# Optimization experiments

Measured on AMD Instinct MI355X. Metric: run time of the kernel, lower is better.

Reference implementation:

```python
import jax, jax.numpy as jnp
import numpy as np

N = 50000
E = 800000
IN = 128
H = 256


def _sage_conv(x, src, dst, W_l, b_l, W_r, n_nodes):
    # PyG SAGEConv (aggr='mean'): out = lin_l(mean_{j in N(i)} x_j) + lin_r(x_i)
    msg = x[src]                                             # [E, d] gather
    agg = jax.ops.segment_sum(msg, dst, num_segments=n_nodes)  # [N, d]
    cnt = jax.ops.segment_sum(jnp.ones((src.shape[0],), x.dtype), dst,
                              num_segments=n_nodes)
    agg = agg / jnp.maximum(cnt, 1.0)[:, None]               # scatter-mean
    return agg @ W_l + b_l + x @ W_r


def setup_inputs() -> dict:
    key = jax.random.key(0)
    ks = jax.random.split(key, 12)
    s_in, s_h, s_h2 = 1.0 / np.sqrt(IN), 1.0 / np.sqrt(H), 1.0 / np.sqrt(H // 2)
    return {
        "x": jax.random.normal(ks[0], (N, IN), jnp.float32),
        "edge_index": jax.random.randint(ks[1], (2, E), 0, N, dtype=jnp.int32),
        # conv1: in -> H
        "W1_l": jax.random.uniform(ks[2], (IN, H), jnp.float32, -s_in, s_in),
        "b1_l": jnp.zeros((H,), jnp.float32),
        "W1_r": jax.random.uniform(ks[3], (IN, H), jnp.float32, -s_in, s_in),
        # conv2: H -> H
        "W2_l": jax.random.uniform(ks[4], (H, H), jnp.float32, -s_h, s_h),
        "b2_l": jnp.zeros((H,), jnp.float32),
        "W2_r": jax.random.uniform(ks[5], (H, H), jnp.float32, -s_h, s_h),
        # risk head: H -> H//2 -> 1
        "Wh1": jax.random.uniform(ks[6], (H, H // 2), jnp.float32, -s_h, s_h),
        "bh1": jax.random.uniform(ks[7], (H // 2,), jnp.float32, -s_h, s_h),
        "Wh2": jax.random.uniform(ks[8], (H // 2, 1), jnp.float32, -s_h2, s_h2),
        "bh2": jax.random.uniform(ks[9], (1,), jnp.float32, -s_h2, s_h2),
    }


def reference(x, edge_index, W1_l, b1_l, W1_r, W2_l, b2_l, W2_r,
              Wh1, bh1, Wh2, bh2):
    src, dst = edge_index[0], edge_index[1]
    h = jax.nn.relu(_sage_conv(x, src, dst, W1_l, b1_l, W1_r, N))
    h = jax.nn.relu(_sage_conv(h, src, dst, W2_l, b2_l, W2_r, N))
    # risk head (dropout is identity in inference)
    h = jax.nn.relu(h @ Wh1 + bh1)
    return jax.nn.sigmoid(h @ Wh2 + bh2)            # [N, 1]
```

## Files before the change

### kernel.cpp

```cpp
#include <hip/hip_runtime.h>
#include <cstdint>
#include <cstddef>

#define N_NODES 50000
#define N_EDGES 800000
#define DIM_IN 128
#define DIM_H 256
#define CAP 64

using u16 = unsigned short;
using u32 = unsigned int;
using u8 = unsigned char;

typedef __attribute__((ext_vector_type(8))) short bf16x8;
typedef __attribute__((ext_vector_type(4))) float f32x4;
typedef __attribute__((ext_vector_type(2))) float f32x2;

__device__ __forceinline__ u16 f2bf(float x) {
    u32 u = __float_as_uint(x);
    u32 r = (u + 0x7fffu + ((u >> 16) & 1u)) >> 16;
    return (u16)r;
}

__device__ __forceinline__ u8 enc1_sw(float f) {
    u32 u = __float_as_uint(f);
    u32 s = (u >> 24) & 0x80u;
    u32 a = u & 0x7fffffffu;
    if (a >= 0x43e00000u) return (u8)(s | 0x7e);
    if (a < 0x3c800000u) return (u8)s;
    u32 r = a + 0x7ffffu + ((a >> 20) & 1u);
    u32 e8 = (r >> 23) - 120u;
    if (e8 >= 16u) return (u8)(s | 0x7e);
    return (u8)(s | (e8 << 3) | ((r >> 20) & 7u));
}

__device__ __forceinline__ u32 enc4(float f0, float f1, float f2, float f3) {
#if __has_builtin(__builtin_amdgcn_cvt_pk_fp8_f32)
    int w = __builtin_amdgcn_cvt_pk_fp8_f32(f0, f1, 0, false);
    w = __builtin_amdgcn_cvt_pk_fp8_f32(f2, f3, w, true);
    return (u32)w;
#else
    return (u32)enc1_sw(f0) | ((u32)enc1_sw(f1) << 8) |
           ((u32)enc1_sw(f2) << 16) | ((u32)enc1_sw(f3) << 24);
#endif
}

__device__ __forceinline__ u8 enc1(float f) {
#if __has_builtin(__builtin_amdgcn_cvt_pk_fp8_f32)
    return (u8)(__builtin_amdgcn_cvt_pk_fp8_f32(f, 0.f, 0, false) & 0xff);
#else
    return enc1_sw(f);
#endif
}

__device__ __forceinline__ void dec_u32(float* o, u32 w) {
#if __has_builtin(__builtin_amdgcn_cvt_pk_f32_fp8)
    f32x2 a = __builtin_amdgcn_cvt_pk_f32_fp8(w, false);
    f32x2 b = __builtin_amdgcn_cvt_pk_f32_fp8(w, true);
    o[0] = a[0]; o[1] = a[1]; o[2] = b[0]; o[3] = b[1];
#else
    #pragma unroll
    for (int k = 0; k < 4; ++k) {
        u32 x = (w >> (8 * k)) & 0xffu;
        u32 bits = ((x & 0x80u) << 24) | ((x & 0x7fu) << 20);
        o[k] = __uint_as_float(bits) * __uint_as_float(0x7b800000u);
    }
#endif
}

__device__ __forceinline__ void gld_lds16(const u16* g, u16* l) {
    __builtin_amdgcn_global_load_lds(
        (__attribute__((address_space(1))) void*)g,
        (__attribute__((address_space(3))) void*)l, 16, 0, 0);
}

__global__ void fill_bucket(const int* __restrict__ src, const int* __restrict__ dst,
                            int* __restrict__ cnt, int* __restrict__ csr, int e) {
    int i = blockIdx.x * blockDim.x + threadIdx.x;
    if (i < e) {
        int d = dst[i];
        int slot = atomicAdd(&cnt[d], 1);
        if (slot < CAP) csr[d * CAP + slot] = src[i];
    }
}

__global__ __launch_bounds__(256) void prep(
    const float* __restrict__ x,
    const float* __restrict__ W1_l, const float* __restrict__ W1_r,
    const float* __restrict__ W2_l, const float* __restrict__ W2_r,
    const float* __restrict__ Wh1,
    u16* __restrict__ x_hi, u32* __restrict__ x_f8,
    u16* __restrict__ w1l, u16* __restrict__ w1r,
    u16* __restrict__ w2l, u16* __restrict__ w2r, u16* __restrict__ wh1,
    int* __restrict__ cnt) {
    int b = blockIdx.x, tid = threadIdx.x;
    if (b < 49) {
        int i = b * 256 + tid;
        if (i < 12500) reinterpret_cast<int4*>(cnt)[i] = make_int4(0, 0, 0, 0);
        return;
    }
    b -= 49;
    if (b < 6250) {
        int i = b * 256 + tid;
        float4 v = reinterpret_cast<const float4*>(x)[i];
        ushort4 h;
        h.x = f2bf(v.x); h.y = f2bf(v.y); h.z = f2bf(v.z); h.w = f2bf(v.w);
        reinterpret_cast<ushort4*>(x_hi)[i] = h;
        x_f8[i] = enc4(v.x, v.y, v.z, v.w);
        return;
    }
    b -= 6250;
    if (b < 128) {
        int idx = b * 256 + tid; int m = idx >> 7, k = idx & 127;
        w1l[idx] = f2bf(W1_l[(size_t)k * 256 + m]); return;
    }
    b -= 128;
    if (b < 128) {
        int idx = b * 256 + tid; int m = idx >> 7, k = idx & 127;
        w1r[idx] = f2bf(W1_r[(size_t)k * 256 + m]); return;
    }
    b -= 128;
    if (b < 256) {
        int idx = b * 256 + tid; int m = idx >> 8, k = idx & 255;
        w2l[idx] = f2bf(W2_l[(size_t)k * 256 + m]); return;
    }
    b -= 256;
    if (b < 256) {
        int idx = b * 256 + tid; int m = idx >> 8, k = idx & 255;
        w2r[idx] = f2bf(W2_r[(size_t)k * 256 + m]); return;
    }
    b -= 256;
    {
        int idx = b * 256 + tid; int m = idx >> 8, k = idx & 255;
        wh1[idx] = f2bf(Wh1[(size_t)k * 128 + m]);
    }
}

__device__ __forceinline__ void acc16_add(float* acc, uint4 a) {
    float t[4];
    dec_u32(t, a.x); acc[0] += t[0]; acc[1] += t[1]; acc[2] += t[2]; acc[3] += t[3];
    dec_u32(t, a.y); acc[4] += t[0]; acc[5] += t[1]; acc[6] += t[2]; acc[7] += t[3];
    dec_u32(t, a.z); acc[8] += t[0]; acc[9] += t[1]; acc[10] += t[2]; acc[11] += t[3];
    dec_u32(t, a.w); acc[12] += t[0]; acc[13] += t[1]; acc[14] += t[2]; acc[15] += t[3];
}

template <int U4ROW>
__global__ __launch_bounds__(256) void aggregate_f8(
    const uint4* __restrict__ tab, const int* __restrict__ cnt,
    const int* __restrict__ csr, u16* __restrict__ out_hi, int n_nodes) {
    constexpr int EPI = 64 / U4ROW;
    constexpr int D = U4ROW * 16;
    const int lane = threadIdx.x & 63;
    const int v = blockIdx.x * 4 + (threadIdx.x >> 6);
    if (v >= n_nodes) return;
    const int q = lane & (U4ROW - 1);
    const int e = lane / U4ROW;
    const int d = cnt[v];
    const int dl = min(d, CAP);
    const int myidx = (lane < dl) ? csr[v * CAP + lane] : 0;
    float acc[16] = {};
    int j = 0;
    for (; j + 2 * EPI <= dl; j += 2 * EPI) {
        int i0 = __shfl(myidx, j + e, 64);
        int i1 = __shfl(myidx, j + EPI + e, 64);
        uint4 a = tab[(size_t)i0 * U4ROW + q];
        uint4 b = tab[(size_t)i1 * U4ROW + q];
        acc16_add(acc, a);
        acc16_add(acc, b);
    }
    for (; j + EPI <= dl; j += EPI) {
        int i0 = __shfl(myidx, j + e, 64);
        uint4 a = tab[(size_t)i0 * U4ROW + q];
        acc16_add(acc, a);
    }
    int r = dl - j;
    if (r > 0) {
        int ee = (e < r) ? e : 0;
        int i0 = __shfl(myidx, j + ee, 64);
        uint4 a = tab[(size_t)i0 * U4ROW + q];
        if (e < r) acc16_add(acc, a);
    }
    #pragma unroll
    for (int s = U4ROW; s < 64; s <<= 1)
        #pragma unroll
        for (int i = 0; i < 16; ++i) acc[i] += __shfl_xor(acc[i], s, 64);
    const float inv = 1.f / (float)((d > 0) ? d : 1);
    if (e == 0) {
        u32 w[8];
        #pragma unroll
        for (int k = 0; k < 8; ++k) {
            float m0 = acc[2 * k] * inv, m1 = acc[2 * k + 1] * inv;
            w[k] = ((u32)f2bf(m1) << 16) | f2bf(m0);
        }
        u16* dp = out_hi + (size_t)v * D + q * 16;
        *reinterpret_cast<uint4*>(dp) = *reinterpret_cast<uint4*>(&w[0]);
        *reinterpret_cast<uint4*>(dp + 8) = *reinterpret_cast<uint4*>(&w[4]);
    }
}

template <int MODE>
__global__ __launch_bounds__(512) void gemm_fused(
    const u16* __restrict__ Ah1, const u16* __restrict__ Ah2,
    const u16* __restrict__ Bh1, const u16* __restrict__ Bh2,
    const float* __restrict__ bias,
    const u16* __restrict__ wh1t, const float* __restrict__ bh1,
    const float* __restrict__ wh2, const float* __restrict__ bh2,
    u16* __restrict__ Chi, u8* __restrict__ Cf8, float* __restrict__ outF,
    int nrows, int K) {
    __shared__ u16 SMEM[(MODE == 1) ? 37888 : 12288];
    u16* As = SMEM;
    u16* Bs = SMEM + 4096;

    const int tid = threadIdx.x;
    const int lane = tid & 63;
    const int w = tid >> 6;
    const int wr = w >> 2, wc = w & 3;
    const int row0 = blockIdx.x * 128;

    const u16* const Aph[2] = {Ah1, Ah2};
    const u16* const Bph[2] = {Bh1, Bh2};

    f32x4 zero4 = {0.f, 0.f, 0.f, 0.f};
    f32x4 acc[4][4];
    #pragma unroll
    for (int i = 0; i < 4; ++i)
        #pragma unroll
        for (int j = 0; j < 4; ++j) acc[i][j] = zero4;

    const int srow = lane >> 2;
    const int schunk = (lane & 3) * 8;

    const int nks = K >> 5;
    for (int ph = 0; ph < 2; ++ph) {
        const u16* Ab = Aph[ph];
        const u16* Bb = Bph[ph];
        for (int kk = 0; kk < nks; ++kk) {
            #pragma unroll
            for (int t = 0; t < 3; ++t) {
                int slab = w * 3 + t;
                if (slab < 8) {
                    int grow = row0 + slab * 16 + srow;
                    if (grow > nrows - 1) grow = nrows - 1;
                    gld_lds16(Ab + (size_t)grow * K + kk * 32 + schunk,
                              As + slab * 512);
                } else {
                    int gcol = (slab - 8) * 16 + srow;
                    gld_lds16(Bb + (size_t)gcol * K + kk * 32 + schunk,
                              Bs + (slab - 8) * 512);
                }
            }
            __syncthreads();
            bf16x8 af[4], bfr[4];
            #pragma unroll
            for (int i = 0; i < 4; ++i)
                af[i] = *reinterpret_cast<const bf16x8*>(
                    &As[(wr * 64 + i * 16 + (lane & 15)) * 32 + (lane >> 4) * 8]);
            #pragma unroll
            for (int j = 0; j < 4; ++j)
                bfr[j] = *reinterpret_cast<const bf16x8*>(
                    &Bs[(wc * 64 + j * 16 + (lane & 15)) * 32 + (lane >> 4) * 8]);
            #pragma unroll
            for (int i = 0; i < 4; ++i)
                #pragma unroll
                for (int j = 0; j < 4; ++j)
                    acc[i][j] = __builtin_amdgcn_mfma_f32_16x16x32_bf16(
                        af[i], bfr[j], acc[i][j], 0, 0, 0);
            __syncthreads();
        }
    }

    if (MODE == 0) {
        #pragma unroll
        for (int i = 0; i < 4; ++i) {
            #pragma unroll
            for (int j = 0; j < 4; ++j) {
                int col = wc * 64 + j * 16 + (lane & 15);
                float b = bias[col];
                #pragma unroll
                for (int r = 0; r < 4; ++r) {
                    int row = row0 + wr * 64 + i * 16 + (lane >> 4) * 4 + r;
                    if (row < nrows) {
                        float v = fmaxf(acc[i][j][r] + b, 0.f);
                        Chi[(size_t)row * 256 + col] = f2bf(v);
                        Cf8[(size_t)row * 256 + col] = enc1(v);
                    }
                }
            }
        }
    } else {
        char* hb = (char*)SMEM;
        #pragma unroll
        for (int i = 0; i < 4; ++i)
            #pragma unroll
            for (int j = 0; j < 4; ++j) {
                int col = wc * 64 + j * 16 + (lane & 15);
                float b = bias[col];
                #pragma unroll
                for (int r = 0; r < 4; ++r) {
                    int row = wr * 64 + i * 16 + (lane >> 4) * 4 + r;
                    float v = fmaxf(acc[i][j][r] + b, 0.f);
                    int byt = row * 512 + col * 2;
                    *(u16*)(hb + (byt ^ ((row & 7) << 4))) = f2bf(v);
                }
            }
        __syncthreads();

        u16* Bs2 = SMEM + 32768;
        float* hpart = (float*)(SMEM + 32768 + 4096);
        const int whr = wr, whc = wc;
        f32x4 acc2[4][2];
        #pragma unroll
        for (int i = 0; i < 4; ++i) {
            acc2[i][0] = zero4; acc2[i][1] = zero4;
        }
        for (int kk = 0; kk < 8; ++kk) {
            {
                int gcol = w * 16 + srow;
                gld_lds16(wh1t + (size_t)gcol * 256 + kk * 32 + schunk,
                          Bs2 + w * 512);
            }
            __syncthreads();
            bf16x8 af2[4], bfr2[2];
            #pragma unroll
            for (int i = 0; i < 4; ++i) {
                int row = whr * 64 + i * 16 + (lane & 15);
                int byt = row * 512 + kk * 64 + (lane >> 4) * 16;
                af2[i] = *reinterpret_cast<const bf16x8*>(hb + (byt ^ ((row & 7) << 4)));
            }
            #pragma unroll
            for (int j = 0; j < 2; ++j)
                bfr2[j] = *reinterpret_cast<const bf16x8*>(
                    &Bs2[(whc * 32 + j * 16 + (lane & 15)) * 32 + (lane >> 4) * 8]);
            #pragma unroll
            for (int i = 0; i < 4; ++i)
                #pragma unroll
                for (int j = 0; j < 2; ++j)
                    acc2[i][j] = __builtin_amdgcn_mfma_f32_16x16x32_bf16(
                        af2[i], bfr2[j], acc2[i][j], 0, 0, 0);
            __syncthreads();
        }

        float pr[4][4];
        #pragma unroll
        for (int i = 0; i < 4; ++i)
            #pragma unroll
            for (int r = 0; r < 4; ++r) pr[i][r] = 0.f;
        #pragma unroll
        for (int j = 0; j < 2; ++j) {
            int col = whc * 32 + j * 16 + (lane & 15);
            float b1 = bh1[col];
            float wv = wh2[col];
            #pragma unroll
            for (int i = 0; i < 4; ++i)
                #pragma unroll
                for (int r = 0; r < 4; ++r)
                    pr[i][r] += fmaxf(acc2[i][j][r] + b1, 0.f) * wv;
        }
        #pragma unroll
        for (int i = 0; i < 4; ++i)
            #pragma unroll
            for (int r = 0; r < 4; ++r) {
                float s = pr[i][r];
                s += __shfl_xor(s, 1, 64);
                s += __shfl_xor(s, 2, 64);
                s += __shfl_xor(s, 4, 64);
                s += __shfl_xor(s, 8, 64);
                pr[i][r] = s;
            }
        if ((lane & 15) == 0) {
            #pragma unroll
            for (int i = 0; i < 4; ++i)
                #pragma unroll
                for (int r = 0; r < 4; ++r)
                    hpart[whc * 128 + whr * 64 + i * 16 + (lane >> 4) * 4 + r] = pr[i][r];
        }
        __syncthreads();
        if (tid < 128) {
            int row = row0 + tid;
            if (row < nrows) {
                float s = hpart[tid] + hpart[128 + tid] + hpart[256 + tid]
                        + hpart[384 + tid] + bh2[0];
                outF[row] = 1.f / (1.f + expf(-s));
            }
        }
    }
}

static inline size_t align256(size_t x) { return (x + 255) & ~(size_t)255; }

extern "C" void kernel_launch(void* const* d_in, const int* in_sizes, int n_in,
                              void* d_out, int out_size, void* d_ws, size_t ws_size,
                              hipStream_t stream) {
    const float* x    = (const float*)d_in[0];
    const int* ei     = (const int*)d_in[1];
    const float* W1_l = (const float*)d_in[2];
    const float* b1_l = (const float*)d_in[3];
    const float* W1_r = (const float*)d_in[4];
    const float* W2_l = (const float*)d_in[5];
    const float* b2_l = (const float*)d_in[6];
    const float* W2_r = (const float*)d_in[7];
    const float* Wh1  = (const float*)d_in[8];
    const float* bh1  = (const float*)d_in[9];
    const float* Wh2  = (const float*)d_in[10];
    const float* bh2  = (const float*)d_in[11];
    float* out = (float*)d_out;

    const int* src = ei;
    const int* dst = ei + N_EDGES;

    const size_t SZ_N128 = (size_t)N_NODES * DIM_IN * sizeof(u16);
    const size_t SZ_N256 = (size_t)N_NODES * DIM_H * sizeof(u16);
    const size_t SZ_W128x256 = (size_t)128 * 256 * sizeof(u16);

    char* ws = (char*)d_ws;
    size_t off_ = 0;
    auto alloc = [&](size_t bytes) { size_t o = off_; off_ += align256(bytes); return o; };

    size_t o_cnt = alloc((size_t)N_NODES * 4);
    size_t o_csr = alloc((size_t)N_NODES * CAP * 4);
    size_t o_w1l = alloc(SZ_W128x256);
    size_t o_w1r = alloc(SZ_W128x256);
    size_t o_w2l = alloc(2 * SZ_W128x256);
    size_t o_w2r = alloc(2 * SZ_W128x256);
    size_t o_wh1 = alloc(SZ_W128x256);
    size_t o_xh  = alloc(SZ_N128);
    size_t o_xf8 = alloc((size_t)N_NODES * DIM_IN);
    size_t o_a1  = alloc(SZ_N128);
    size_t o_h1  = alloc(SZ_N256);
    size_t o_h1f = alloc((size_t)N_NODES * DIM_H);
    size_t o_a2  = alloc(SZ_N256);
    if (ws_size < off_) return;

    int* cnt = (int*)(ws + o_cnt);
    int* csr = (int*)(ws + o_csr);
    u16* w1l_h = (u16*)(ws + o_w1l);
    u16* w1r_h = (u16*)(ws + o_w1r);
    u16* w2l_h = (u16*)(ws + o_w2l);
    u16* w2r_h = (u16*)(ws + o_w2r);
    u16* wh1_h = (u16*)(ws + o_wh1);
    u16* x_hi    = (u16*)(ws + o_xh);
    u32* x_f8    = (u32*)(ws + o_xf8);
    u16* agg1_hi = (u16*)(ws + o_a1);
    u16* h1_hi   = (u16*)(ws + o_h1);
    u8*  h1_f8   = (u8*)(ws + o_h1f);
    u16* agg2_hi = (u16*)(ws + o_a2);

    prep<<<49 + 6250 + 128 + 128 + 256 + 256 + 128, 256, 0, stream>>>(
        x, W1_l, W1_r, W2_l, W2_r, Wh1,
        x_hi, x_f8, w1l_h, w1r_h, w2l_h, w2r_h, wh1_h, cnt);

    fill_bucket<<<(N_EDGES + 255) / 256, 256, 0, stream>>>(src, dst, cnt, csr, N_EDGES);

    const int RB = (N_NODES + 127) / 128;
    const int AB = (N_NODES + 3) / 4;

    aggregate_f8<8><<<AB, 256, 0, stream>>>(
        (const uint4*)x_f8, cnt, csr, agg1_hi, N_NODES);
    gemm_fused<0><<<RB, 512, 0, stream>>>(
        agg1_hi, x_hi, w1l_h, w1r_h, b1_l,
        nullptr, nullptr, nullptr, nullptr, h1_hi, h1_f8, nullptr, N_NODES, 128);

    aggregate_f8<16><<<AB, 256, 0, stream>>>(
        (const uint4*)h1_f8, cnt, csr, agg2_hi, N_NODES);
    gemm_fused<1><<<RB, 512, 0, stream>>>(
        agg2_hi, h1_hi, w2l_h, w2r_h, b2_l,
        wh1_h, bh1, Wh2, bh2, nullptr, nullptr, out, N_NODES, 256);
}
```

Baseline: 174.6 us.

## Replace global-atomic CSR fill with two-pass binned build using LDS atomics

Measured after the change: 153.7 us. 1.14x faster.

```diff
diff --git a/kernel.cpp b/kernel.cpp
--- a/kernel.cpp
+++ b/kernel.cpp
@@ -3,10 +3,15 @@
 #include <cstddef>
 
 #define N_NODES 50000
+#define N_PAD 50048
 #define N_EDGES 800000
 #define DIM_IN 128
 #define DIM_H 256
 #define CAP 64
+#define NBKT 391
+#define BCAP 2560
+#define BINA_BLOCKS 400
+#define EPB 2000
 
 using u16 = unsigned short;
 using u32 = unsigned int;
@@ -74,13 +79,58 @@
         (__attribute__((address_space(3))) void*)l, 16, 0, 0);
 }
 
-__global__ void fill_bucket(const int* __restrict__ src, const int* __restrict__ dst,
-                            int* __restrict__ cnt, int* __restrict__ csr, int e) {
-    int i = blockIdx.x * blockDim.x + threadIdx.x;
-    if (i < e) {
+__global__ __launch_bounds__(256) void binA(
+    const int* __restrict__ src, const int* __restrict__ dst,
+    int* __restrict__ gcur, int2* __restrict__ binbuf) {
+    __shared__ int hist[NBKT];
+    __shared__ int base[NBKT];
+    const int tid = threadIdx.x;
+    const int e0 = blockIdx.x * EPB;
+    const int e1 = min(e0 + EPB, N_EDGES);
+    for (int t = tid; t < NBKT; t += 256) hist[t] = 0;
+    __syncthreads();
+    for (int i = e0 + tid; i < e1; i += 256)
+        atomicAdd(&hist[dst[i] >> 7], 1);
+    __syncthreads();
+    for (int t = tid; t < NBKT; t += 256) {
+        int h = hist[t];
+        base[t] = h ? atomicAdd(&gcur[t], h) : 0;
+    }
+    __syncthreads();
+    for (int t = tid; t < NBKT; t += 256) hist[t] = 0;
+    __syncthreads();
+    for (int i = e0 + tid; i < e1; i += 256) {
         int d = dst[i];
-        int slot = atomicAdd(&cnt[d], 1);
-        if (slot < CAP) csr[d * CAP + slot] = src[i];
+        int b = d >> 7;
+        int o = base[b] + atomicAdd(&hist[b], 1);
+        if (o < (b + 1) * BCAP) binbuf[o] = make_int2(src[i], d);
+    }
+}
+
+__global__ __launch_bounds__(256) void binB(
+    const int* __restrict__ gcur, const int2* __restrict__ binbuf,
+    int* __restrict__ cnt, int* __restrict__ csr) {
+    __shared__ int lcnt[128];
+    __shared__ int lcsr[128 * CAP];
+    const int b = blockIdx.x;
+    const int tid = threadIdx.x;
+    if (tid < 128) lcnt[tid] = 0;
+    __syncthreads();
+    int gc = gcur[b] - b * BCAP;
+    if (gc > BCAP) gc = BCAP;
+    for (int i = tid; i < gc; i += 256) {
+        int2 p = binbuf[b * BCAP + i];
+        int n = p.y & 127;
+        int slot = atomicAdd(&lcnt[n], 1);
+        if (slot < CAP) lcsr[n * CAP + slot] = p.x;
+    }
+    __syncthreads();
+    const uint4* ls = reinterpret_cast<const uint4*>(lcsr);
+    uint4* gs = reinterpret_cast<uint4*>(csr + (size_t)b * 128 * CAP);
+    for (int i = tid; i < 128 * CAP / 4; i += 256) gs[i] = ls[i];
+    if (tid < 128) {
+        int v = b * 128 + tid;
+        if (v < N_NODES) cnt[v] = lcnt[tid];
     }
 }
 
@@ -92,14 +142,14 @@
     u16* __restrict__ x_hi, u32* __restrict__ x_f8,
     u16* __restrict__ w1l, u16* __restrict__ w1r,
     u16* __restrict__ w2l, u16* __restrict__ w2r, u16* __restrict__ wh1,
-    int* __restrict__ cnt) {
+    int* __restrict__ gcur) {
     int b = blockIdx.x, tid = threadIdx.x;
-    if (b < 49) {
+    if (b < 2) {
         int i = b * 256 + tid;
-        if (i < 12500) reinterpret_cast<int4*>(cnt)[i] = make_int4(0, 0, 0, 0);
+        if (i < NBKT) gcur[i] = i * BCAP;
         return;
     }
-    b -= 49;
+    b -= 2;
     if (b < 6250) {
         int i = b * 256 + tid;
         float4 v = reinterpret_cast<const float4*>(x)[i];
@@ -416,8 +466,10 @@
     size_t off_ = 0;
     auto alloc = [&](size_t bytes) { size_t o = off_; off_ += align256(bytes); return o; };
 
-    size_t o_cnt = alloc((size_t)N_NODES * 4);
-    size_t o_csr = alloc((size_t)N_NODES * CAP * 4);
+    size_t o_cnt = alloc((size_t)N_PAD * 4);
+    size_t o_gcur = alloc((size_t)512 * 4);
+    size_t o_csr = alloc((size_t)N_PAD * CAP * 4);
+    size_t o_bin = alloc((size_t)NBKT * BCAP * 8);
     size_t o_w1l = alloc(SZ_W128x256);
     size_t o_w1r = alloc(SZ_W128x256);
     size_t o_w2l = alloc(2 * SZ_W128x256);
@@ -431,8 +483,10 @@
     size_t o_a2  = alloc(SZ_N256);
     if (ws_size < off_) return;
 
-    int* cnt = (int*)(ws + o_cnt);
-    int* csr = (int*)(ws + o_csr);
+    int* cnt  = (int*)(ws + o_cnt);
+    int* gcur = (int*)(ws + o_gcur);
+    int* csr  = (int*)(ws + o_csr);
+    int2* binbuf = (int2*)(ws + o_bin);
     u16* w1l_h = (u16*)(ws + o_w1l);
     u16* w1r_h = (u16*)(ws + o_w1r);
     u16* w2l_h = (u16*)(ws + o_w2l);
@@ -445,11 +499,12 @@
     u8*  h1_f8   = (u8*)(ws + o_h1f);
     u16* agg2_hi = (u16*)(ws + o_a2);
 
-    prep<<<49 + 6250 + 128 + 128 + 256 + 256 + 128, 256, 0, stream>>>(
+    prep<<<2 + 6250 + 128 + 128 + 256 + 256 + 128, 256, 0, stream>>>(
         x, W1_l, W1_r, W2_l, W2_r, Wh1,
-        x_hi, x_f8, w1l_h, w1r_h, w2l_h, w2r_h, wh1_h, cnt);
-
-    fill_bucket<<<(N_EDGES + 255) / 256, 256, 0, stream>>>(src, dst, cnt, csr, N_EDGES);
+        x_hi, x_f8, w1l_h, w1r_h, w2l_h, w2r_h, wh1_h, gcur);
+
+    binA<<<BINA_BLOCKS, 256, 0, stream>>>(src, dst, gcur, binbuf);
+    binB<<<NBKT, 256, 0, stream>>>(gcur, binbuf, cnt, csr);
 
     const int RB = (N_NODES + 127) / 128;
     const int AB = (N_NODES + 3) / 4;
```
